# Kernel tuning notes

Hardware: AMD Instinct MI355X
Metric: run time of the kernel (lower is better)

## Reference

```python
import jax, jax.numpy as jnp
import numpy as np

N_NODES = 100000
DEG = 16   # regular-graph degree -> every per-node subgraph is a (DEG+1)-node star
DIM = 128


def _crelu(z):
    return (jax.nn.relu(z.real) + 1j * jax.nn.relu(z.imag)).astype(jnp.complex64)


def _evolution_row(deg, tr, ti):
    # get_node_adjacency keeps only edges incident to the center node, so A_i is the
    # star graph K_{1,deg} with the center at index 0 -- identical for every node of a
    # deg-regular graph, so U is computed once.
    n = deg + 1
    A = jnp.zeros((n, n), jnp.complex64).at[0, 1:].set(1.0).at[1:, 0].set(1.0)
    t = (tr + 1j * ti).astype(jnp.complex64)
    G = jax.scipy.linalg.expm(-1j * A * t)
    # torch: sqrt(max eigval of G G^dagger); G G^dagger is Hermitian PSD -> eigvalsh
    s = jnp.sqrt(jnp.max(jnp.linalg.eigvalsh(G @ G.conj().T))).astype(jnp.complex64)
    Lt = G / s
    # np.sqrt on a matrix is ELEMENTWISE sqrt in the torch code -- replicate that
    Rt = jnp.sqrt(jnp.eye(n, dtype=jnp.complex64) - Lt @ (G.conj().T / s))
    # torch converts complex_time via .item() into numpy: no grad through U
    return jax.lax.stop_gradient(Lt[0] + Rt[0])  # (deg+1,) complex row 0 of [[Lt,Rt],[Rt,-Lt]]


def _layer(h, nbrs, Wr, Wi, br, bi, tr, ti, ebr, ebi):
    W = (Wr + 1j * Wi).astype(jnp.complex64)
    b = (br + 1j * bi).astype(jnp.complex64)
    h = _crelu(h @ W.T + b)
    deg = nbrs.shape[1]
    w = _evolution_row(deg, tr, ti)
    # evolved[0] = w[0]*h_i + sum_k w[1+k]*h_{sorted_nbr_k(i)}
    out = w[0] * h
    for k in range(deg):  # fixed small unrolled loop; avoids a [N, deg+1, C] intermediate
        out = out + w[1 + k] * h[nbrs[:, k]]
    return out + (ebr + 1j * ebi).astype(jnp.complex64)


def setup_inputs():
    key = jax.random.key(0)
    ks = jax.random.split(key, 12)
    x = jax.random.normal(ks[0], (N_NODES, DIM), jnp.float32)
    # circulant DEG-regular graph: node i ~ i +/- k (mod N), k=1..DEG/2; each undirected edge once
    K = DEG // 2
    i = np.arange(N_NODES)
    src = np.repeat(i, K)
    dst = ((i[:, None] + np.arange(1, K + 1)[None, :]) % N_NODES).reshape(-1)
    edge_index = jnp.asarray(np.stack([src, dst]), dtype=jnp.int32)
    sc = 0.05
    d = {"x": x, "edge_index": edge_index}
    for l, k0 in ((1, 1), (2, 6)):
        d[f"W{l}r"] = jax.random.normal(ks[k0], (DIM, DIM), jnp.float32) * sc
        d[f"W{l}i"] = jax.random.normal(ks[k0 + 1], (DIM, DIM), jnp.float32) * sc
        d[f"b{l}r"] = jax.random.normal(ks[k0 + 2], (DIM,), jnp.float32) * sc
        d[f"b{l}i"] = jax.random.normal(ks[k0 + 3], (DIM,), jnp.float32) * sc
        d[f"t{l}r"] = jnp.float32(1.0)
        d[f"t{l}i"] = jnp.float32(0.0)
        d[f"eb{l}r"] = jnp.zeros((DIM,), jnp.float32)
        d[f"eb{l}i"] = jnp.zeros((DIM,), jnp.float32)
    return d


def reference(x, edge_index, W1r, W1i, b1r, b1i, t1r, t1i, eb1r, eb1i,
              W2r, W2i, b2r, b2i, t2r, t2i, eb2r, eb2i):
    N = x.shape[0]
    src, dst = edge_index[0], edge_index[1]
    nodes = jnp.concatenate([src, dst])
    nbr = jnp.concatenate([dst, src])
    order = jnp.lexsort((nbr, nodes))        # sorted neighbor list per node
    deg = nodes.shape[0] // N                # regular graph -> static degree
    nbrs = nbr[order].reshape(N, deg)        # [N, DEG]
    h = x.astype(jnp.complex64)              # prepare_complex_input
    h = _layer(h, nbrs, W1r, W1i, b1r, b1i, t1r, t1i, eb1r, eb1i)
    h = _layer(h, nbrs, W2r, W2i, b2r, b2i, t2r, t2i, eb2r, eb2i)
    return h.real                            # output_type='real'
```

## Files before the change

### kernel.cpp

```cpp
#include <hip/hip_runtime.h>
#include <hip/hip_bf16.h>
#include <stdint.h>

typedef __attribute__((ext_vector_type(8))) short bf8_t;
typedef __attribute__((ext_vector_type(4))) float f32x4_t;
typedef __attribute__((ext_vector_type(4))) unsigned short us4_t;

#define MFMA_BF16 __builtin_amdgcn_mfma_f32_16x16x32_bf16

__device__ __forceinline__ unsigned short f2bf(float f) {
  union { float f; unsigned u; } x; x.f = f;
  unsigned r = (x.u + 0x7FFFu + ((x.u >> 16) & 1u)) >> 16;
  return (unsigned short)r;
}
__device__ __forceinline__ float bf2f(unsigned short b) {
  union { unsigned u; float f; } x; x.u = ((unsigned)b) << 16;
  return x.f;
}

__device__ __forceinline__ int xcd_swizzle(int b, int nwg) {
  const int NX = 8;
  int q = nwg / NX, r = nwg % NX;
  int xcd = b % NX, idx = b / NX;
  int start = (xcd < r) ? xcd * (q + 1) : r * (q + 1) + (xcd - r) * q;
  return start + idx;
}

__global__ void compute_wscal(const float* t1r, const float* t1i,
                              const float* t2r, const float* t2i,
                              float* wsc, int deg) {
  if (threadIdx.x != 0 || blockIdx.x != 0) return;
  float r = sqrtf((float)deg);
  for (int l = 0; l < 2; ++l) {
    float tr = l ? t2r[0] : t1r[0];
    float ti = l ? t2i[0] : t1i[0];
    float x = r * tr, y = r * ti;
    float cr = cosf(x) * coshf(y), ci = -sinf(x) * sinhf(y);
    float sr = sinf(x) * coshf(y), si = cosf(x) * sinhf(y);
    float a = cr * cr + ci * ci + sr * sr + si * si;
    float b = -2.0f * (ci * sr - cr * si);
    float s2 = fmaxf(a + fabsf(b), 1.0f);
    float s = sqrtf(s2);
    float l0r = cr / s, l0i = ci / s;
    float l1r = si / (r * s), l1i = -sr / (r * s);
    float q0 = 1.0f - a / s2;
    float r0r = (q0 >= 0.0f) ? sqrtf(q0) : 0.0f;
    float r0i = (q0 >= 0.0f) ? 0.0f : sqrtf(-q0);
    float q1 = -b / (r * s2);
    float r1r = (q1 >= 0.0f) ? sqrtf(q1) : 0.0f;
    float r1i = (q1 >= 0.0f) ? 0.0f : sqrtf(-q1);
    wsc[l * 4 + 0] = l0r + r0r;
    wsc[l * 4 + 1] = l0i + r0i;
    wsc[l * 4 + 2] = l1r + r1r;
    wsc[l * 4 + 3] = l1i + r1i;
  }
}

__device__ __forceinline__ void store_side(int* __restrict__ cnt,
                                           int* __restrict__ nbrs,
                                           int deg, int key, int val) {
  unsigned long long remaining = __ballot(1);
  unsigned long long mymask = 0;
  while (remaining) {
    int lead = __ffsll((long long)remaining) - 1;
    int lkey = __shfl(key, lead);
    unsigned long long m = __ballot(key == lkey);
    if (key == lkey) mymask = m;
    remaining &= ~m;
  }
  const int lane = threadIdx.x & 63;
  const int leader = __ffsll((long long)mymask) - 1;
  int base = 0;
  if (lane == leader) base = atomicAdd(&cnt[key], __popcll(mymask));
  base = __shfl(base, leader);
  const int rank = __popcll(mymask & ((1ull << lane) - 1ull));
  nbrs[(long)key * deg + base + rank] = val;
}

__global__ __launch_bounds__(256) void build_nbrs(
    const int* __restrict__ ei, int E, int* __restrict__ cnt,
    int* __restrict__ nbrs, int deg) {
  int e = blockIdx.x * 256 + threadIdx.x;
  if (e >= E) return;
  int s = ei[e], d = ei[E + e];
  store_side(cnt, nbrs, deg, s, d);
  store_side(cnt, nbrs, deg, d, s);
}

__device__ __forceinline__ void stage_w(unsigned char* ldsW,
                                        const float* __restrict__ Wr,
                                        const float* __restrict__ Wi, int tid) {
#pragma unroll
  for (int p = 0; p < 2; ++p) {
    const float* src = p ? Wi : Wr;
#pragma unroll
    for (int i = 0; i < 4; ++i) {
      const int e8 = (i * 512 + tid) * 8;
      float4 a = *(const float4*)(src + e8);
      float4 b = *(const float4*)(src + e8 + 4);
      union { bf8_t v; unsigned short s[8]; } o;
      o.s[0] = f2bf(a.x); o.s[1] = f2bf(a.y); o.s[2] = f2bf(a.z); o.s[3] = f2bf(a.w);
      o.s[4] = f2bf(b.x); o.s[5] = f2bf(b.y); o.s[6] = f2bf(b.z); o.s[7] = f2bf(b.w);
      const int c = e8 >> 7, k = e8 & 127;
      const int byte = p * 32768 + c * 256 + ((k * 2) ^ ((c & 7) << 4));
      *(bf8_t*)(ldsW + byte) = o.v;
    }
  }
}


__global__ __launch_bounds__(512) void gemm_l1(
    const float* __restrict__ Xf,
    const float* __restrict__ Wr, const float* __restrict__ Wi,
    const float* __restrict__ br, const float* __restrict__ bi,
    unsigned short* __restrict__ H1, int n) {
  __shared__ unsigned char ldsW[65536];
  const int tid = threadIdx.x;
  stage_w(ldsW, Wr, Wi, tid);
  __syncthreads();

  const int wv = tid >> 6, lane = tid & 63;
  const int fr = lane & 15, kg = lane >> 4;
  const int lb = xcd_swizzle(blockIdx.x, gridDim.x);
  const int rowbase = lb * 128 + wv * 16;
  const int node = min(rowbase + fr, n - 1);
  const long a_off = (long)node * 128;

  bf8_t a[4];
#pragma unroll
  for (int ks = 0; ks < 4; ++ks) {
    const int koff = ks * 32 + kg * 8;
    float4 u = *(const float4*)(Xf + a_off + koff);
    float4 v = *(const float4*)(Xf + a_off + koff + 4);
    union { bf8_t vv; unsigned short s[8]; } t;
    t.s[0] = f2bf(u.x); t.s[1] = f2bf(u.y); t.s[2] = f2bf(u.z); t.s[3] = f2bf(u.w);
    t.s[4] = f2bf(v.x); t.s[5] = f2bf(v.y); t.s[6] = f2bf(v.z); t.s[7] = f2bf(v.w);
    a[ks] = t.vv;
  }

  const int onode = rowbase + fr;
  const long obase = (long)onode * 256;
#pragma unroll
  for (int cf = 0; cf < 8; ++cf) {
    const int c = cf * 16 + fr;
    const int cbyte = c * 256, swz = (c & 7) << 4;
    f32x4_t accr = (f32x4_t)0.0f, acci = (f32x4_t)0.0f;
#pragma unroll
    for (int ks = 0; ks < 4; ++ks) {
      const int kb = (ks * 32 + kg * 8) * 2;
      bf8_t w_r = *(const bf8_t*)(ldsW + cbyte + (kb ^ swz));
      bf8_t w_i = *(const bf8_t*)(ldsW + 32768 + cbyte + (kb ^ swz));
      accr = MFMA_BF16(w_r, a[ks], accr, 0, 0, 0);
      acci = MFMA_BF16(w_i, a[ks], acci, 0, 0, 0);
    }
    if (onode < n) {
      const int cb = cf * 16 + kg * 4;
      const int chunk = cb >> 3, sub = cb & 7;
      union { float4 f4; float f[4]; } b4r, b4i;
      b4r.f4 = *(const float4*)(br + cb);
      b4i.f4 = *(const float4*)(bi + cb);
      us4_t pr, pi;
#pragma unroll
      for (int j = 0; j < 4; ++j) {
        pr[j] = f2bf(fmaxf(accr[j] + b4r.f[j], 0.0f));
        pi[j] = f2bf(fmaxf(acci[j] + b4i.f[j], 0.0f));
      }
      *(us4_t*)(H1 + obase + chunk * 16 + sub) = pr;
      *(us4_t*)(H1 + obase + chunk * 16 + 8 + sub) = pi;
    }
  }
}

template <int DEG>
__global__ __launch_bounds__(512) void fused_l2(
    const unsigned short* __restrict__ H1,
    const int* __restrict__ nbrs, const float* __restrict__ wsc,
    const float* __restrict__ eb1r, const float* __restrict__ eb1i,
    const float* __restrict__ W2r, const float* __restrict__ W2i,
    const float* __restrict__ b2r, const float* __restrict__ b2i,
    unsigned short* __restrict__ H2, int n, int deg_rt) {
  __shared__ unsigned char ldsW[65536];
  const int tid = threadIdx.x;
  stage_w(ldsW, W2r, W2i, tid);
  __syncthreads();

  const int wv = tid >> 6, lane = tid & 63;
  const int fr = lane & 15, kg = lane >> 4;
  const int lb = xcd_swizzle(blockIdx.x, gridDim.x);
  const int rowbase = lb * 128 + wv * 16;
  const int node = min(rowbase + fr, n - 1);
  const float w0r = wsc[0], w0i = wsc[1], w1r = wsc[2], w1i = wsc[3];
  const int deg = DEG ? DEG : deg_rt;
  const int* nbp = nbrs + (long)node * deg;

  int nb[DEG ? DEG : 1];
  if (DEG) {
#pragma unroll
    for (int j = 0; j < (DEG ? DEG : 1); ++j) nb[j] = nbp[j];
  }

  bf8_t ar[4], ai[4], ain[4];
#pragma unroll
  for (int ks = 0; ks < 4; ++ks) {
    const int ch16 = (ks * 4 + kg) * 16;
    union { bf8_t v; unsigned short s[8]; } o_r, o_i;
    o_r.v = *(const bf8_t*)(H1 + (long)node * 256 + ch16);
    o_i.v = *(const bf8_t*)(H1 + (long)node * 256 + ch16 + 8);
    float sr[8], si[8];
#pragma unroll
    for (int e = 0; e < 8; ++e) { sr[e] = 0.0f; si[e] = 0.0f; }
    if (DEG) {
#pragma unroll
      for (int j = 0; j < (DEG ? DEG : 1); ++j) {
        const long m = (long)nb[j] * 256 + ch16;
        union { bf8_t v; unsigned short s[8]; } vr2, vi2;
        vr2.v = *(const bf8_t*)(H1 + m);
        vi2.v = *(const bf8_t*)(H1 + m + 8);
#pragma unroll
        for (int e = 0; e < 8; ++e) { sr[e] += bf2f(vr2.s[e]); si[e] += bf2f(vi2.s[e]); }
      }
    } else {
      for (int j = 0; j < deg; ++j) {
        const long m = (long)nbp[j] * 256 + ch16;
        union { bf8_t v; unsigned short s[8]; } vr2, vi2;
        vr2.v = *(const bf8_t*)(H1 + m);
        vi2.v = *(const bf8_t*)(H1 + m + 8);
#pragma unroll
        for (int e = 0; e < 8; ++e) { sr[e] += bf2f(vr2.s[e]); si[e] += bf2f(vi2.s[e]); }
      }
    }
    const int koff = ks * 32 + kg * 8;
    union { float4 f4; float f[4]; } er0, er1, ei0, ei1;
    er0.f4 = *(const float4*)(eb1r + koff);
    er1.f4 = *(const float4*)(eb1r + koff + 4);
    ei0.f4 = *(const float4*)(eb1i + koff);
    ei1.f4 = *(const float4*)(eb1i + koff + 4);
    union { bf8_t v; unsigned short s[8]; } pr, pi;
#pragma unroll
    for (int e = 0; e < 8; ++e) {
      float hr = bf2f(o_r.s[e]), hi = bf2f(o_i.s[e]);
      float ebR = (e < 4) ? er0.f[e] : er1.f[e - 4];
      float ebI = (e < 4) ? ei0.f[e] : ei1.f[e - 4];
      float gr = w0r * hr - w0i * hi + w1r * sr[e] - w1i * si[e] + ebR;
      float gi = w0r * hi + w0i * hr + w1r * si[e] + w1i * sr[e] + ebI;
      pr.s[e] = f2bf(gr); pi.s[e] = f2bf(gi);
    }
    ar[ks] = pr.v; ai[ks] = pi.v;
    union { bf8_t v; unsigned u[4]; } t; t.v = pi.v;
#pragma unroll
    for (int q = 0; q < 4; ++q) t.u[q] ^= 0x80008000u;
    ain[ks] = t.v;
  }

  const int onode = rowbase + fr;
  const long obase = (long)onode * 256;
#pragma unroll
  for (int cf = 0; cf < 8; ++cf) {
    const int c = cf * 16 + fr;
    const int cbyte = c * 256, swz = (c & 7) << 4;
    f32x4_t accr = (f32x4_t)0.0f, acci = (f32x4_t)0.0f;
#pragma unroll
    for (int ks = 0; ks < 4; ++ks) {
      const int kb = (ks * 32 + kg * 8) * 2;
      bf8_t w_r = *(const bf8_t*)(ldsW + cbyte + (kb ^ swz));
      bf8_t w_i = *(const bf8_t*)(ldsW + 32768 + cbyte + (kb ^ swz));
      accr = MFMA_BF16(w_r, ar[ks], accr, 0, 0, 0);
      accr = MFMA_BF16(w_i, ain[ks], accr, 0, 0, 0);
      acci = MFMA_BF16(w_i, ar[ks], acci, 0, 0, 0);
      acci = MFMA_BF16(w_r, ai[ks], acci, 0, 0, 0);
    }
    if (onode < n) {
      const int cb = cf * 16 + kg * 4;
      const int chunk = cb >> 3, sub = cb & 7;
      union { float4 f4; float f[4]; } b4r, b4i;
      b4r.f4 = *(const float4*)(b2r + cb);
      b4i.f4 = *(const float4*)(b2i + cb);
      us4_t pr, pi;
#pragma unroll
      for (int j = 0; j < 4; ++j) {
        pr[j] = f2bf(fmaxf(accr[j] + b4r.f[j], 0.0f));
        pi[j] = f2bf(fmaxf(acci[j] + b4i.f[j], 0.0f));
      }
      *(us4_t*)(H2 + obase + chunk * 16 + sub) = pr;
      *(us4_t*)(H2 + obase + chunk * 16 + 8 + sub) = pi;
    }
  }
}

template <int DEG>
__global__ __launch_bounds__(256) void agg_final(
    const unsigned short* __restrict__ H2,
    const int* __restrict__ nbrs, const float* __restrict__ wsc,
    const float* __restrict__ ebr,
    float* __restrict__ outf, int n, int deg_rt) {
  const int lb = xcd_swizzle(blockIdx.x, gridDim.x);
  const int g = lb * 256 + threadIdx.x;
  const int node = g >> 4;
  if (node >= n) return;
  const int g2 = g & 15;
  const int ch0 = g2 * 8;
  const int deg = DEG ? DEG : deg_rt;
  const float w0r = wsc[0], w0i = wsc[1], w1r = wsc[2], w1i = wsc[3];

  union { bf8_t v; unsigned short s[8]; } ur, ui;
  ur.v = *(const bf8_t*)(H2 + (long)node * 256 + g2 * 16);
  ui.v = *(const bf8_t*)(H2 + (long)node * 256 + g2 * 16 + 8);
  float srf[8], sif[8];
#pragma unroll
  for (int e = 0; e < 8; ++e) { srf[e] = 0.0f; sif[e] = 0.0f; }
  const int* nbp = nbrs + (long)node * deg;
  if (DEG) {
#pragma unroll
    for (int k = 0; k < (DEG ? DEG : 1); ++k) {
      const long m = (long)nbp[k] * 256 + g2 * 16;
      union { bf8_t v; unsigned short s[8]; } vr2, vi2;
      vr2.v = *(const bf8_t*)(H2 + m);
      vi2.v = *(const bf8_t*)(H2 + m + 8);
#pragma unroll
      for (int e = 0; e < 8; ++e) { srf[e] += bf2f(vr2.s[e]); sif[e] += bf2f(vi2.s[e]); }
    }
  } else {
    for (int k = 0; k < deg; ++k) {
      const long m = (long)nbp[k] * 256 + g2 * 16;
      union { bf8_t v; unsigned short s[8]; } vr2, vi2;
      vr2.v = *(const bf8_t*)(H2 + m);
      vi2.v = *(const bf8_t*)(H2 + m + 8);
#pragma unroll
      for (int e = 0; e < 8; ++e) { srf[e] += bf2f(vr2.s[e]); sif[e] += bf2f(vi2.s[e]); }
    }
  }
  union { float4 f4; float f[4]; } o0, o1;
#pragma unroll
  for (int e = 0; e < 8; ++e) {
    const int c = ch0 + e;
    float hrf = bf2f(ur.s[e]), hif = bf2f(ui.s[e]);
    float R = w0r * hrf - w0i * hif + w1r * srf[e] - w1i * sif[e] + ebr[c];
    if (e < 4) o0.f[e] = R; else o1.f[e - 4] = R;
  }
  *(float4*)(outf + (long)node * 128 + ch0) = o0.f4;
  *(float4*)(outf + (long)node * 128 + ch0 + 4) = o1.f4;
}

extern "C" void kernel_launch(void* const* d_in, const int* in_sizes, int n_in,
                              void* d_out, int out_size, void* d_ws, size_t ws_size,
                              hipStream_t stream) {
  const float* x    = (const float*)d_in[0];
  const int*   ei   = (const int*)d_in[1];
  const float* W1r  = (const float*)d_in[2];
  const float* W1i  = (const float*)d_in[3];
  const float* b1r  = (const float*)d_in[4];
  const float* b1i  = (const float*)d_in[5];
  const float* t1r  = (const float*)d_in[6];
  const float* t1i  = (const float*)d_in[7];
  const float* eb1r = (const float*)d_in[8];
  const float* eb1i = (const float*)d_in[9];
  const float* W2r  = (const float*)d_in[10];
  const float* W2i  = (const float*)d_in[11];
  const float* b2r  = (const float*)d_in[12];
  const float* b2i  = (const float*)d_in[13];
  const float* t2r  = (const float*)d_in[14];
  const float* t2i  = (const float*)d_in[15];
  const float* eb2r = (const float*)d_in[16];
  const float* eb2i = (const float*)d_in[17];

  const int DIM = 128;
  const int N = in_sizes[0] / DIM;
  const int E = in_sizes[1] / 2;
  const int deg = (2 * E) / N;

  char* ws = (char*)d_ws;
  size_t off = 0;
  auto alloc = [&](size_t bytes) -> char* {
    char* p = ws + off;
    off += (bytes + 255) & ~(size_t)255;
    return p;
  };
  int* cnt  = (int*)alloc((size_t)N * 4);
  int* nbrs = (int*)alloc((size_t)N * deg * 4);
  float* wsc = (float*)alloc(8 * 4);
  const size_t nH = (size_t)N * DIM;
  unsigned short* h1 = (unsigned short*)alloc(nH * 4);
  unsigned short* h2 = (unsigned short*)alloc(nH * 4);
  (void)ws_size; (void)n_in; (void)out_size;

  hipMemsetAsync(cnt, 0, (size_t)N * 4, stream);
  build_nbrs<<<(E + 255) / 256, 256, 0, stream>>>(ei, E, cnt, nbrs, deg);
  compute_wscal<<<1, 64, 0, stream>>>(t1r, t1i, t2r, t2i, wsc, deg);

  const int gemm_blocks = (N + 127) / 128;
  const int agg_blocks = (N * 16 + 255) / 256;

  gemm_l1<<<gemm_blocks, 512, 0, stream>>>(x, W1r, W1i, b1r, b1i, h1, N);

  if (deg == 16) {
    fused_l2<16><<<gemm_blocks, 512, 0, stream>>>(h1, nbrs, wsc, eb1r, eb1i,
                                                  W2r, W2i, b2r, b2i, h2, N, deg);
    agg_final<16><<<agg_blocks, 256, 0, stream>>>(h2, nbrs, wsc + 4, eb2r,
                                                  (float*)d_out, N, deg);
  } else {
    fused_l2<0><<<gemm_blocks, 512, 0, stream>>>(h1, nbrs, wsc, eb1r, eb1i,
                                                 W2r, W2i, b2r, b2i, h2, N, deg);
    agg_final<0><<<agg_blocks, 256, 0, stream>>>(h2, nbrs, wsc + 4, eb2r,
                                                 (float*)d_out, N, deg);
  }
}
```

Baseline: 338.8 us.

## Halve LDS weight staging via two-pass real/imag planes and stage neighbor lists in LDS

Both GEMM kernels now keep only one 32KB bf16 weight plane in LDS at a time. They compute the real-weight contributions into per-fragment accumulators, then restage the imaginary plane and finish. With __launch_bounds__(512,4) this is meant to allow more resident blocks per CU so more of the gather latency can be hidden. fused_l2 also loads the block's neighbor indices cooperatively into padded LDS instead of per-thread register loads. The cost is extra barriers, a second staging pass, and 64 live accumulator floats per thread, which could cause register pressure or spills.

Result: slower. 386.4 us (+14.1%).

```diff
diff --git a/kernel.cpp b/kernel.cpp
--- a/kernel.cpp
+++ b/kernel.cpp
@@ -87,44 +87,39 @@
   store_side(cnt, nbrs, deg, d, s);
 }
 
-__device__ __forceinline__ void stage_w(unsigned char* ldsW,
-                                        const float* __restrict__ Wr,
-                                        const float* __restrict__ Wi, int tid) {
-#pragma unroll
-  for (int p = 0; p < 2; ++p) {
-    const float* src = p ? Wi : Wr;
-#pragma unroll
-    for (int i = 0; i < 4; ++i) {
-      const int e8 = (i * 512 + tid) * 8;
-      float4 a = *(const float4*)(src + e8);
-      float4 b = *(const float4*)(src + e8 + 4);
-      union { bf8_t v; unsigned short s[8]; } o;
-      o.s[0] = f2bf(a.x); o.s[1] = f2bf(a.y); o.s[2] = f2bf(a.z); o.s[3] = f2bf(a.w);
-      o.s[4] = f2bf(b.x); o.s[5] = f2bf(b.y); o.s[6] = f2bf(b.z); o.s[7] = f2bf(b.w);
-      const int c = e8 >> 7, k = e8 & 127;
-      const int byte = p * 32768 + c * 256 + ((k * 2) ^ ((c & 7) << 4));
-      *(bf8_t*)(ldsW + byte) = o.v;
-    }
-  }
-}
-
-
-__global__ __launch_bounds__(512) void gemm_l1(
+__device__ __forceinline__ void stage_w_plane(unsigned char* ldsW,
+                                              const float* __restrict__ src,
+                                              int tid) {
+#pragma unroll
+  for (int i = 0; i < 4; ++i) {
+    const int e8 = (i * 512 + tid) * 8;
+    float4 a = *(const float4*)(src + e8);
+    float4 b = *(const float4*)(src + e8 + 4);
+    union { bf8_t v; unsigned short s[8]; } o;
+    o.s[0] = f2bf(a.x); o.s[1] = f2bf(a.y); o.s[2] = f2bf(a.z); o.s[3] = f2bf(a.w);
+    o.s[4] = f2bf(b.x); o.s[5] = f2bf(b.y); o.s[6] = f2bf(b.z); o.s[7] = f2bf(b.w);
+    const int c = e8 >> 7, k = e8 & 127;
+    const int byte = c * 256 + ((k * 2) ^ ((c & 7) << 4));
+    *(bf8_t*)(ldsW + byte) = o.v;
+  }
+}
+
+
+__global__ __launch_bounds__(512, 4) void gemm_l1(
     const float* __restrict__ Xf,
     const float* __restrict__ Wr, const float* __restrict__ Wi,
     const float* __restrict__ br, const float* __restrict__ bi,
     unsigned short* __restrict__ H1, int n) {
-  __shared__ unsigned char ldsW[65536];
+  __shared__ unsigned char ldsW[32768];
   const int tid = threadIdx.x;
-  stage_w(ldsW, Wr, Wi, tid);
-  __syncthreads();
-
   const int wv = tid >> 6, lane = tid & 63;
   const int fr = lane & 15, kg = lane >> 4;
   const int lb = xcd_swizzle(blockIdx.x, gridDim.x);
   const int rowbase = lb * 128 + wv * 16;
   const int node = min(rowbase + fr, n - 1);
   const long a_off = (long)node * 128;
+
+  stage_w_plane(ldsW, Wr, tid);
 
   bf8_t a[4];
 #pragma unroll
@@ -137,23 +132,43 @@
     t.s[4] = f2bf(v.x); t.s[5] = f2bf(v.y); t.s[6] = f2bf(v.z); t.s[7] = f2bf(v.w);
     a[ks] = t.vv;
   }
-
-  const int onode = rowbase + fr;
-  const long obase = (long)onode * 256;
+  __syncthreads();
+
+  f32x4_t accr[8], acci[8];
+#pragma unroll
+  for (int i = 0; i < 8; ++i) { accr[i] = (f32x4_t)0.0f; acci[i] = (f32x4_t)0.0f; }
+
 #pragma unroll
   for (int cf = 0; cf < 8; ++cf) {
     const int c = cf * 16 + fr;
     const int cbyte = c * 256, swz = (c & 7) << 4;
-    f32x4_t accr = (f32x4_t)0.0f, acci = (f32x4_t)0.0f;
 #pragma unroll
     for (int ks = 0; ks < 4; ++ks) {
       const int kb = (ks * 32 + kg * 8) * 2;
-      bf8_t w_r = *(const bf8_t*)(ldsW + cbyte + (kb ^ swz));
-      bf8_t w_i = *(const bf8_t*)(ldsW + 32768 + cbyte + (kb ^ swz));
-      accr = MFMA_BF16(w_r, a[ks], accr, 0, 0, 0);
-      acci = MFMA_BF16(w_i, a[ks], acci, 0, 0, 0);
-    }
-    if (onode < n) {
+      bf8_t w = *(const bf8_t*)(ldsW + cbyte + (kb ^ swz));
+      accr[cf] = MFMA_BF16(w, a[ks], accr[cf], 0, 0, 0);
+    }
+  }
+  __syncthreads();
+  stage_w_plane(ldsW, Wi, tid);
+  __syncthreads();
+#pragma unroll
+  for (int cf = 0; cf < 8; ++cf) {
+    const int c = cf * 16 + fr;
+    const int cbyte = c * 256, swz = (c & 7) << 4;
+#pragma unroll
+    for (int ks = 0; ks < 4; ++ks) {
+      const int kb = (ks * 32 + kg * 8) * 2;
+      bf8_t w = *(const bf8_t*)(ldsW + cbyte + (kb ^ swz));
+      acci[cf] = MFMA_BF16(w, a[ks], acci[cf], 0, 0, 0);
+    }
+  }
+
+  const int onode = rowbase + fr;
+  if (onode < n) {
+    const long obase = (long)onode * 256;
+#pragma unroll
+    for (int cf = 0; cf < 8; ++cf) {
       const int cb = cf * 16 + kg * 4;
       const int chunk = cb >> 3, sub = cb & 7;
       union { float4 f4; float f[4]; } b4r, b4i;
@@ -162,8 +177,8 @@
       us4_t pr, pi;
 #pragma unroll
       for (int j = 0; j < 4; ++j) {
-        pr[j] = f2bf(fmaxf(accr[j] + b4r.f[j], 0.0f));
-        pi[j] = f2bf(fmaxf(acci[j] + b4i.f[j], 0.0f));
+        pr[j] = f2bf(fmaxf(accr[cf][j] + b4r.f[j], 0.0f));
+        pi[j] = f2bf(fmaxf(acci[cf][j] + b4i.f[j], 0.0f));
       }
       *(us4_t*)(H1 + obase + chunk * 16 + sub) = pr;
       *(us4_t*)(H1 + obase + chunk * 16 + 8 + sub) = pi;
@@ -172,34 +187,39 @@
 }
 
 template <int DEG>
-__global__ __launch_bounds__(512) void fused_l2(
+__global__ __launch_bounds__(512, 4) void fused_l2(
     const unsigned short* __restrict__ H1,
     const int* __restrict__ nbrs, const float* __restrict__ wsc,
     const float* __restrict__ eb1r, const float* __restrict__ eb1i,
     const float* __restrict__ W2r, const float* __restrict__ W2i,
     const float* __restrict__ b2r, const float* __restrict__ b2i,
     unsigned short* __restrict__ H2, int n, int deg_rt) {
-  __shared__ unsigned char ldsW[65536];
+  __shared__ unsigned char ldsW[32768];
+  __shared__ int ldsNB[128 * 17];
   const int tid = threadIdx.x;
-  stage_w(ldsW, W2r, W2i, tid);
-  __syncthreads();
-
   const int wv = tid >> 6, lane = tid & 63;
   const int fr = lane & 15, kg = lane >> 4;
   const int lb = xcd_swizzle(blockIdx.x, gridDim.x);
   const int rowbase = lb * 128 + wv * 16;
   const int node = min(rowbase + fr, n - 1);
+  const int nloc = wv * 16 + fr;
   const float w0r = wsc[0], w0i = wsc[1], w1r = wsc[2], w1i = wsc[3];
   const int deg = DEG ? DEG : deg_rt;
-  const int* nbp = nbrs + (long)node * deg;
-
-  int nb[DEG ? DEG : 1];
-  if (DEG) {
-#pragma unroll
-    for (int j = 0; j < (DEG ? DEG : 1); ++j) nb[j] = nbp[j];
-  }
-
-  bf8_t ar[4], ai[4], ain[4];
+
+  {
+    const long base = (long)lb * 128 * deg;
+    const long lim = (long)n * deg;
+    for (int i = tid; i < 128 * deg; i += 512) {
+      long gidx = base + i;
+      int v = (gidx < lim) ? nbrs[gidx] : 0;
+      v = min(max(v, 0), n - 1);
+      ldsNB[(i / deg) * 17 + (i % deg)] = v;
+    }
+  }
+  stage_w_plane(ldsW, W2r, tid);
+  __syncthreads();
+
+  bf8_t ar[4], ai[4];
 #pragma unroll
   for (int ks = 0; ks < 4; ++ks) {
     const int ch16 = (ks * 4 + kg) * 16;
@@ -209,19 +229,10 @@
     float sr[8], si[8];
 #pragma unroll
     for (int e = 0; e < 8; ++e) { sr[e] = 0.0f; si[e] = 0.0f; }
-    if (DEG) {
-#pragma unroll
-      for (int j = 0; j < (DEG ? DEG : 1); ++j) {
-        const long m = (long)nb[j] * 256 + ch16;
-        union { bf8_t v; unsigned short s[8]; } vr2, vi2;
-        vr2.v = *(const bf8_t*)(H1 + m);
-        vi2.v = *(const bf8_t*)(H1 + m + 8);
-#pragma unroll
-        for (int e = 0; e < 8; ++e) { sr[e] += bf2f(vr2.s[e]); si[e] += bf2f(vi2.s[e]); }
-      }
-    } else {
-      for (int j = 0; j < deg; ++j) {
-        const long m = (long)nbp[j] * 256 + ch16;
+#pragma unroll
+    for (int j = 0; j < (DEG ? DEG : 1); ++j) {
+      for (int jj = DEG ? j : 0; jj < (DEG ? j + 1 : deg); ++jj) {
+        const long m = (long)ldsNB[nloc * 17 + jj] * 256 + ch16;
         union { bf8_t v; unsigned short s[8]; } vr2, vi2;
         vr2.v = *(const bf8_t*)(H1 + m);
         vi2.v = *(const bf8_t*)(H1 + m + 8);
@@ -246,30 +257,53 @@
       pr.s[e] = f2bf(gr); pi.s[e] = f2bf(gi);
     }
     ar[ks] = pr.v; ai[ks] = pi.v;
-    union { bf8_t v; unsigned u[4]; } t; t.v = pi.v;
-#pragma unroll
-    for (int q = 0; q < 4; ++q) t.u[q] ^= 0x80008000u;
-    ain[ks] = t.v;
-  }
-
-  const int onode = rowbase + fr;
-  const long obase = (long)onode * 256;
+  }
+
+  f32x4_t accr[8], acci[8];
+#pragma unroll
+  for (int i = 0; i < 8; ++i) { accr[i] = (f32x4_t)0.0f; acci[i] = (f32x4_t)0.0f; }
+
 #pragma unroll
   for (int cf = 0; cf < 8; ++cf) {
     const int c = cf * 16 + fr;
     const int cbyte = c * 256, swz = (c & 7) << 4;
-    f32x4_t accr = (f32x4_t)0.0f, acci = (f32x4_t)0.0f;
 #pragma unroll
     for (int ks = 0; ks < 4; ++ks) {
       const int kb = (ks * 32 + kg * 8) * 2;
-      bf8_t w_r = *(const bf8_t*)(ldsW + cbyte + (kb ^ swz));
-      bf8_t w_i = *(const bf8_t*)(ldsW + 32768 + cbyte + (kb ^ swz));
-      accr = MFMA_BF16(w_r, ar[ks], accr, 0, 0, 0);
-      accr = MFMA_BF16(w_i, ain[ks], accr, 0, 0, 0);
-      acci = MFMA_BF16(w_i, ar[ks], acci, 0, 0, 0);
-      acci = MFMA_BF16(w_r, ai[ks], acci, 0, 0, 0);
-    }
-    if (onode < n) {
+      bf8_t w = *(const bf8_t*)(ldsW + cbyte + (kb ^ swz));
+      accr[cf] = MFMA_BF16(w, ar[ks], accr[cf], 0, 0, 0);
+      acci[cf] = MFMA_BF16(w, ai[ks], acci[cf], 0, 0, 0);
+    }
+  }
+  __syncthreads();
+  stage_w_plane(ldsW, W2i, tid);
+  __syncthreads();
+
+#pragma unroll
+  for (int ks = 0; ks < 4; ++ks) {
+    union { bf8_t v; unsigned u[4]; } t; t.v = ai[ks];
+#pragma unroll
+    for (int q = 0; q < 4; ++q) t.u[q] ^= 0x80008000u;
+    ai[ks] = t.v;
+  }
+#pragma unroll
+  for (int cf = 0; cf < 8; ++cf) {
+    const int c = cf * 16 + fr;
+    const int cbyte = c * 256, swz = (c & 7) << 4;
+#pragma unroll
+    for (int ks = 0; ks < 4; ++ks) {
+      const int kb = (ks * 32 + kg * 8) * 2;
+      bf8_t w = *(const bf8_t*)(ldsW + cbyte + (kb ^ swz));
+      accr[cf] = MFMA_BF16(w, ai[ks], accr[cf], 0, 0, 0);
+      acci[cf] = MFMA_BF16(w, ar[ks], acci[cf], 0, 0, 0);
+    }
+  }
+
+  const int onode = rowbase + fr;
+  if (onode < n) {
+    const long obase = (long)onode * 256;
+#pragma unroll
+    for (int cf = 0; cf < 8; ++cf) {
       const int cb = cf * 16 + kg * 4;
       const int chunk = cb >> 3, sub = cb & 7;
       union { float4 f4; float f[4]; } b4r, b4i;
@@ -278,8 +312,8 @@
       us4_t pr, pi;
 #pragma unroll
       for (int j = 0; j < 4; ++j) {
-        pr[j] = f2bf(fmaxf(accr[j] + b4r.f[j], 0.0f));
-        pi[j] = f2bf(fmaxf(acci[j] + b4i.f[j], 0.0f));
+        pr[j] = f2bf(fmaxf(accr[cf][j] + b4r.f[j], 0.0f));
+        pi[j] = f2bf(fmaxf(acci[cf][j] + b4i.f[j], 0.0f));
       }
       *(us4_t*)(H2 + obase + chunk * 16 + sub) = pr;
       *(us4_t*)(H2 + obase + chunk * 16 + 8 + sub) = pi;
@@ -309,19 +343,10 @@
 #pragma unroll
   for (int e = 0; e < 8; ++e) { srf[e] = 0.0f; sif[e] = 0.0f; }
   const int* nbp = nbrs + (long)node * deg;
-  if (DEG) {
-#pragma unroll
-    for (int k = 0; k < (DEG ? DEG : 1); ++k) {
-      const long m = (long)nbp[k] * 256 + g2 * 16;
-      union { bf8_t v; unsigned short s[8]; } vr2, vi2;
-      vr2.v = *(const bf8_t*)(H2 + m);
-      vi2.v = *(const bf8_t*)(H2 + m + 8);
-#pragma unroll
-      for (int e = 0; e < 8; ++e) { srf[e] += bf2f(vr2.s[e]); sif[e] += bf2f(vi2.s[e]); }
-    }
-  } else {
-    for (int k = 0; k < deg; ++k) {
-      const long m = (long)nbp[k] * 256 + g2 * 16;
+#pragma unroll
+  for (int k = 0; k < (DEG ? DEG : 1); ++k) {
+    for (int kk = DEG ? k : 0; kk < (DEG ? k + 1 : deg); ++kk) {
+      const long m = (long)nbp[kk] * 256 + g2 * 16;
       union { bf8_t v; unsigned short s[8]; } vr2, vi2;
       vr2.v = *(const bf8_t*)(H2 + m);
       vi2.v = *(const bf8_t*)(H2 + m + 8);
```
